# Kernel tuning notes

Measured on AMD Instinct MI355X. Metric: run time of the kernel, lower is better.

Reference implementation:

```python
import jax, jax.numpy as jnp
import numpy as np

B, GRID, D, NF, NC = 4096, 8, 64, 256, 10
N = GRID * GRID          # num_nodes = grid_size**2
LN_EPS = 1e-5            # torch LayerNorm default eps


def _grid_mask():
    m = np.zeros((N, N), np.float32)
    for i in range(N):
        r, c = divmod(i, GRID)
        if r > 0: m[i, i - GRID] = 1
        if r < GRID - 1: m[i, i + GRID] = 1
        if c > 0: m[i, i - 1] = 1
        if c < GRID - 1: m[i, i + 1] = 1
    return jnp.asarray(m)

MASK = _grid_mask()  # static 4-neighbor grid adjacency mask [N,N]


def _ln(x, g, b):
    mu = x.mean(-1, keepdims=True)
    v = ((x - mu) ** 2).mean(-1, keepdims=True)  # biased var, like torch LayerNorm
    return (x - mu) / jnp.sqrt(v + LN_EPS) * g + b


def _regulator(x, h_pre, w_norm, p):
    # HomeostaticRegulator.forward (eval mode: baselines fixed at 0.5 / 1.0)
    var = jnp.var(x, axis=1, ddof=1, keepdims=True)            # torch.var default unbiased=True
    natural_stress = jnp.abs(var - 0.5)
    xs = jnp.sort(x, axis=1)
    smoothness = jnp.abs(xs[:, 1:] - xs[:, :-1]).mean(1, keepdims=True)
    adversarial_stress = jnp.abs(smoothness - 1.0)
    excitation = jnp.abs(h_pre).mean(1, keepdims=True)
    fatigue = jnp.broadcast_to(jnp.reshape(w_norm, (1, 1)), (x.shape[0], 1))
    gradient_proxy = jnp.sqrt((h_pre ** 2).mean(1, keepdims=True))
    s = jnp.concatenate([natural_stress, adversarial_stress, excitation, fatigue, gradient_proxy], axis=1)
    h = jnp.tanh(_ln(s @ p[0].T + p[1], p[2], p[3]))
    h = jnp.tanh(_ln(h @ p[4].T + p[5], p[6], p[7]))
    return jax.nn.sigmoid(h @ p[8].T + p[9])  # [B,3] = metabolism, sensitivity, gate


def _cell(x, W_slow, W_fast, ln_g, ln_b, cp):
    # HomeoContinuumCell.forward, eval mode (no Hebbian buffer update)
    h_raw = jax.lax.stop_gradient(x @ W_slow.T)                 # computed under torch.no_grad
    w_norm = jax.lax.stop_gradient(jnp.sqrt((W_slow ** 2).sum()))
    ctl = _regulator(x, h_raw, w_norm, cp)
    beta = 0.5 + ctl[:, 1:2] * 2.0
    gate = ctl[:, 2:3]
    comb = x @ W_slow.T + (x @ W_fast.T) * gate
    act = comb * jax.nn.sigmoid(beta * comb)
    return _ln(act, ln_g, ln_b)


def _forward(x, W_embed, b_embed, adj_weights, W_slow, W_fast, ln_g, ln_b, W_read, b_read, tp, cp):
    e = x @ W_embed.T + b_embed                                 # [B, N*D]
    e3 = e.reshape(B, N, D)
    # HomeoTopology.get_adjacency with homeostasis (all under no_grad in torch)
    ts = jax.lax.stop_gradient(e.reshape(1, -1))                # flatten whole batch state
    wn = jax.lax.stop_gradient(jnp.sqrt((adj_weights ** 2).sum()))
    ctl = jax.lax.stop_gradient(_regulator(ts, ts, wn, tp))
    ap = ctl[:, 0].mean()                                       # plasticity(=1.0) * mean metabolism
    adj = jax.nn.sigmoid(adj_weights * ap) * MASK
    adj = adj / jnp.clip(adj.sum(1, keepdims=True), 1e-6, None)
    m = jnp.einsum('nm,bmd->bnd', adj, e3)                      # grid message passing
    proc = _cell(m.reshape(B * N, D), W_slow, W_fast, ln_g, ln_b, cp)
    return proc.reshape(B, N * D) @ W_read.T + b_read           # logits [B, NC]


def _reg_params(key, scale=0.2):
    ks = jax.random.split(key, 3)
    return (jax.random.normal(ks[0], (16, 5)) * scale, jnp.zeros(16), jnp.ones(16), jnp.zeros(16),
            jax.random.normal(ks[1], (8, 16)) * scale, jnp.zeros(8), jnp.ones(8), jnp.zeros(8),
            jax.random.normal(ks[2], (3, 8)) * scale, jnp.zeros(3))


def setup_inputs() -> dict:
    key = jax.random.key(0)
    ks = jax.random.split(key, 9)
    inp = {
        'x': jax.random.normal(ks[0], (B, NF)),
        'W_embed': jax.random.normal(ks[1], (N * D, NF)) * (1.0 / np.sqrt(NF)),
        'b_embed': jnp.zeros(N * D),
        'adj_weights': jax.random.normal(ks[2], (N, N)) * 0.1,
        'W_slow': jax.random.normal(ks[3], (D, D)) * (1.4 / np.sqrt(D)),
        'W_fast': jax.random.normal(ks[4], (D, D)) * 0.05,
        'ln_g': jnp.ones(D), 'ln_b': jnp.zeros(D),
        'W_read': jax.random.normal(ks[5], (NC, N * D)) * (1.0 / np.sqrt(N * D)),
        'b_read': jnp.zeros(NC),
    }
    names = ['W1', 'b1', 'g1', 'bb1', 'W2', 'b2', 'g2', 'bb2', 'W3', 'b3']
    for pre, k in (('t', ks[6]), ('c', ks[7])):
        for n, v in zip(names, _reg_params(k)):
            inp[pre + '_' + n] = v
    return inp


def reference(x, W_embed, b_embed, adj_weights, W_slow, W_fast, ln_g, ln_b, W_read, b_read,
              t_W1, t_b1, t_g1, t_bb1, t_W2, t_b2, t_g2, t_bb2, t_W3, t_b3,
              c_W1, c_b1, c_g1, c_bb1, c_W2, c_b2, c_g2, c_bb2, c_W3, c_b3):
    tp = (t_W1, t_b1, t_g1, t_bb1, t_W2, t_b2, t_g2, t_bb2, t_W3, t_b3)
    cp = (c_W1, c_b1, c_g1, c_bb1, c_W2, c_b2, c_g2, c_bb2, c_W3, c_b3)
    return _forward(x, W_embed, b_embed, adj_weights, W_slow, W_fast, ln_g, ln_b, W_read, b_read, tp, cp)
```

## Files before the change

### kernel.cpp

```cpp
#include <hip/hip_runtime.h>

typedef unsigned short u16;
typedef unsigned int   u32;
typedef float f32x4 __attribute__((ext_vector_type(4)));
typedef int   i32x4 __attribute__((ext_vector_type(4)));
typedef int   i32x2 __attribute__((ext_vector_type(2)));
typedef short s8v   __attribute__((ext_vector_type(8)));

__device__ inline u16 f2bf(float f) {
  u32 u = __float_as_uint(f);
  return (u16)((u + 0x7FFFu + ((u >> 16) & 1u)) >> 16);
}
__device__ inline float bf2f(u16 h) { return __uint_as_float(((u32)h) << 16); }

__device__ inline u32 fkey(float f) {
  u32 u = __float_as_uint(f);
  return (u & 0x80000000u) ? ~u : (u | 0x80000000u);
}
__device__ inline float unkey(u32 k) {
  u32 u = (k & 0x80000000u) ? (k & 0x7FFFFFFFu) : ~k;
  return __uint_as_float(u);
}
__device__ inline float fast_tanh(float x) {
  float cx = fminf(fmaxf(x, -15.f), 15.f);
  float e = __expf(2.f * cx);
  return __fdividef(e - 1.f, e + 1.f);
}
__device__ inline float sigm(float x) { return __fdividef(1.f, 1.f + __expf(-x)); }

__device__ inline void gload_lds16(const u16* g, u16* l) {
  __builtin_amdgcn_global_load_lds((const __attribute__((address_space(1))) u32*)g,
                                   (__attribute__((address_space(3))) u32*)l, 16, 0, 0);
}

struct MlpP { const float *W1,*b1,*g1,*bb1,*W2,*b2,*g2,*bb2,*W3,*b3; };

__device__ inline void mlp_eval(const MlpP& p, const float* s, float* ctl) {
  float h1[16];
  float mu = 0.f;
  #pragma unroll
  for (int i = 0; i < 16; ++i) {
    float v = p.b1[i];
    #pragma unroll
    for (int k = 0; k < 5; ++k) v = fmaf(p.W1[i*5+k], s[k], v);
    h1[i] = v; mu += v;
  }
  mu *= (1.0f/16.0f);
  float vv = 0.f;
  #pragma unroll
  for (int i = 0; i < 16; ++i) { float d = h1[i]-mu; vv += d*d; }
  vv *= (1.0f/16.0f);
  float inv = 1.0f/sqrtf(vv + 1e-5f);
  #pragma unroll
  for (int i = 0; i < 16; ++i) h1[i] = fast_tanh((h1[i]-mu)*inv*p.g1[i] + p.bb1[i]);
  float h2[8];
  mu = 0.f;
  #pragma unroll
  for (int o = 0; o < 8; ++o) {
    float v = p.b2[o];
    #pragma unroll
    for (int i = 0; i < 16; ++i) v = fmaf(p.W2[o*16+i], h1[i], v);
    h2[o] = v; mu += v;
  }
  mu *= 0.125f;
  vv = 0.f;
  #pragma unroll
  for (int o = 0; o < 8; ++o) { float d = h2[o]-mu; vv += d*d; }
  vv *= 0.125f;
  inv = 1.0f/sqrtf(vv + 1e-5f);
  #pragma unroll
  for (int o = 0; o < 8; ++o) h2[o] = fast_tanh((h2[o]-mu)*inv*p.g2[o] + p.bb2[o]);
  #pragma unroll
  for (int c = 0; c < 3; ++c) {
    float v = p.b3[c];
    #pragma unroll
    for (int o = 0; o < 8; ++o) v = fmaf(p.W3[c*8+o], h2[o], v);
    ctl[c] = sigm(v);
  }
}

__global__ __launch_bounds__(256) void k_pre(const float* __restrict__ x,
                                             const float* __restrict__ We,
                                             const float* __restrict__ Ws,
                                             const float* __restrict__ Wf,
                                             u16* __restrict__ Xb, u16* __restrict__ Wb,
                                             u16* __restrict__ WsB, u16* __restrict__ WfB,
                                             float* __restrict__ S) {
  const int bi = blockIdx.x, t = threadIdx.x;
  if (bi < 2048) {
    const float* src = (bi < 1024) ? x : We;
    u16* dst = (bi < 1024) ? Xb : Wb;
    int i = ((bi & 1023) * 256 + t) * 4;
    f32x4 v = *(const f32x4*)(src + i);
    u16 o[4] = { f2bf(v[0]), f2bf(v[1]), f2bf(v[2]), f2bf(v[3]) };
    *(u32*)(dst + i)     = ((u32)o[1] << 16) | o[0];
    *(u32*)(dst + i + 2) = ((u32)o[3] << 16) | o[2];
  } else {
    #pragma unroll
    for (int m = 0; m < 2; ++m) {
      const float* src = m ? Wf : Ws;
      u16* dst = m ? WfB : WsB;
      int base = t * 16;
      u16 o[16];
      #pragma unroll
      for (int r = 0; r < 4; ++r) {
        f32x4 v = *(const f32x4*)(src + base + r*4);
        o[r*4+0]=f2bf(v[0]); o[r*4+1]=f2bf(v[1]); o[r*4+2]=f2bf(v[2]); o[r*4+3]=f2bf(v[3]);
      }
      #pragma unroll
      for (int r = 0; r < 8; ++r)
        *(u32*)(dst + base + r*2) = ((u32)o[r*2+1] << 16) | o[r*2];
    }
    if (t < 3) S[t] = 0.f;
    if (t == 3) ((u32*)S)[3] = 0xFFFFFFFFu;
    if (t == 4) ((u32*)S)[4] = 0u;
  }
}

__global__ __launch_bounds__(256) void k_gemm(const u16* __restrict__ Xb,
                                              const u16* __restrict__ Wb,
                                              const float* __restrict__ bias,
                                              u16* __restrict__ E,
                                              float* __restrict__ S) {
  __shared__ __align__(16) u16 As[2][8192];
  __shared__ __align__(16) u16 Bs[2][8192];
  const int t = threadIdx.x;
  const int wv = t >> 6, lane = t & 63;
  const int wr = wv >> 1, wc = wv & 1;
  const int bid = blockIdx.x;
  const int sw = (bid & 7) * 128 + (bid >> 3);
  const int i0 = (sw >> 5) * 128, j0 = (sw & 31) * 128;
  const int rr = lane & 15, q = lane >> 4;
  const int lrow = lane >> 3, lcol = (lane & 7) * 8;

  f32x4 acc[4][4] = {};
  #pragma unroll
  for (int r = 0; r < 4; ++r) {
    const int row = (r*4 + wv)*8 + lrow;
    gload_lds16(Xb + (size_t)(i0 + row)*256 + lcol, &As[0][(r*4 + wv)*512]);
    gload_lds16(Wb + (size_t)(j0 + row)*256 + lcol, &Bs[0][(r*4 + wv)*512]);
  }
  __syncthreads();
  for (int it = 0; it < 4; ++it) {
    const int cur = it & 1;
    if (it < 3) {
      const int k0 = (it + 1) * 64;
      #pragma unroll
      for (int r = 0; r < 4; ++r) {
        const int row = (r*4 + wv)*8 + lrow;
        gload_lds16(Xb + (size_t)(i0 + row)*256 + k0 + lcol, &As[cur^1][(r*4 + wv)*512]);
        gload_lds16(Wb + (size_t)(j0 + row)*256 + k0 + lcol, &Bs[cur^1][(r*4 + wv)*512]);
      }
    }
    #pragma unroll
    for (int ks = 0; ks < 2; ++ks) {
      s8v a[4], b[4];
      #pragma unroll
      for (int m = 0; m < 4; ++m) a[m] = *(const s8v*)&As[cur][(wr*64 + m*16 + rr)*64 + ks*32 + q*8];
      #pragma unroll
      for (int n = 0; n < 4; ++n) b[n] = *(const s8v*)&Bs[cur][(wc*64 + n*16 + rr)*64 + ks*32 + q*8];
      #pragma unroll
      for (int m = 0; m < 4; ++m)
        #pragma unroll
        for (int n = 0; n < 4; ++n)
          acc[m][n] = __builtin_amdgcn_mfma_f32_16x16x32_bf16(a[m], b[n], acc[m][n], 0, 0, 0);
    }
    __syncthreads();
  }
  float s = 0.f, ss = 0.f, sa = 0.f, mnv = 1e30f, mxv = -1e30f;
  #pragma unroll
  for (int n = 0; n < 4; ++n) {
    const int col = j0 + wc*64 + n*16 + rr;
    const float bv = bias[col];
    #pragma unroll
    for (int m = 0; m < 4; ++m) {
      const int rowb = i0 + wr*64 + m*16 + q*4;
      #pragma unroll
      for (int r = 0; r < 4; ++r) {
        float v = acc[m][n][r] + bv;
        E[(size_t)(rowb + r)*4096 + col] = f2bf(v);
        s += v; ss = fmaf(v, v, ss); sa += fabsf(v);
        mnv = fminf(mnv, v); mxv = fmaxf(mxv, v);
      }
    }
  }
  #pragma unroll
  for (int off = 32; off; off >>= 1) {
    s += __shfl_xor(s, off); ss += __shfl_xor(ss, off); sa += __shfl_xor(sa, off);
    mnv = fminf(mnv, __shfl_xor(mnv, off));
    mxv = fmaxf(mxv, __shfl_xor(mxv, off));
  }
  __shared__ float red5[4][5];
  if (lane == 0) { red5[wv][0]=s; red5[wv][1]=ss; red5[wv][2]=sa; red5[wv][3]=mnv; red5[wv][4]=mxv; }
  __syncthreads();
  if (t == 0) {
    float S0 = red5[0][0]+red5[1][0]+red5[2][0]+red5[3][0];
    float S1 = red5[0][1]+red5[1][1]+red5[2][1]+red5[3][1];
    float S2 = red5[0][2]+red5[1][2]+red5[2][2]+red5[3][2];
    float Mn = fminf(fminf(red5[0][3],red5[1][3]), fminf(red5[2][3],red5[3][3]));
    float Mx = fmaxf(fmaxf(red5[0][4],red5[1][4]), fmaxf(red5[2][4],red5[3][4]));
    atomicAdd(&S[0], S0); atomicAdd(&S[1], S1); atomicAdd(&S[2], S2);
    atomicMin((u32*)S + 3, fkey(Mn));
    atomicMax((u32*)S + 4, fkey(Mx));
  }
}

__global__ __launch_bounds__(256) void k_prep(const float* __restrict__ adjw,
    const float* __restrict__ Wslow,
    const float* tW1, const float* tb1, const float* tg1, const float* tbb1,
    const float* tW2, const float* tb2, const float* tg2, const float* tbb2,
    const float* tW3, const float* tb3,
    float* __restrict__ S) {
  __shared__ float red[2][256];
  __shared__ float apL;
  const int t = threadIdx.x;
  float a = 0.f, w = 0.f;
  for (int i = t; i < 4096; i += 256) {
    float v = adjw[i]; a = fmaf(v, v, a);
    float u = Wslow[i]; w = fmaf(u, u, w);
  }
  red[0][t] = a; red[1][t] = w;
  __syncthreads();
  for (int sred = 128; sred > 0; sred >>= 1) {
    if (t < sred) { red[0][t] += red[0][t+sred]; red[1][t] += red[1][t+sred]; }
    __syncthreads();
  }
  if (t == 0) {
    float wn_t = sqrtf(red[0][0]);
    float wn_c = sqrtf(red[1][0]);
    S[7] = wn_c;
    const float n = 16777216.0f, n1 = 16777215.0f;
    float sum = S[0], sumsq = S[1], sumabs = S[2];
    float mean = sum / n;
    float var = (sumsq - sum*mean) / n1;
    float mn = unkey(((u32*)S)[3]);
    float mx = unkey(((u32*)S)[4]);
    float sfv[5];
    sfv[0] = fabsf(var - 0.5f);
    sfv[1] = fabsf((mx - mn)/n1 - 1.0f);
    sfv[2] = sumabs / n;
    sfv[3] = wn_t;
    sfv[4] = sqrtf(sumsq / n);
    MlpP p{tW1,tb1,tg1,tbb1,tW2,tb2,tg2,tbb2,tW3,tb3};
    float ctl[3];
    mlp_eval(p, sfv, ctl);
    apL = ctl[0];
    S[6] = ctl[0];
  }
  __syncthreads();
  if (t < 64) {
    const int rr = t >> 3, cc = t & 7;
    const float ap = apL;
    const int nb[4] = { rr>0 ? t-8 : -1, rr<7 ? t+8 : -1, cc>0 ? t-1 : -1, cc<7 ? t+1 : -1 };
    float w4[4]; float rs = 0.f;
    #pragma unroll
    for (int qq = 0; qq < 4; ++qq) {
      w4[qq] = (nb[qq] >= 0) ? sigm(adjw[t*64 + nb[qq]] * ap) : 0.0f;
      rs += w4[qq];
    }
    rs = fmaxf(rs, 1e-6f);
    #pragma unroll
    for (int qq = 0; qq < 4; ++qq) S[8 + t*4 + qq] = w4[qq] / rs;
  }
}

__global__ __launch_bounds__(256, 4) void k_cell(const u16* __restrict__ E,
    const u16* __restrict__ WsB, const u16* __restrict__ WfB,
    const float* __restrict__ lng, const float* __restrict__ lnb,
    const float* __restrict__ Wread, const float* __restrict__ bread,
    const float* __restrict__ S,
    const float* cW1, const float* cb1, const float* cg1, const float* cbb1,
    const float* cW2, const float* cb2, const float* cg2, const float* cbb2,
    const float* cW3, const float* cb3,
    float* __restrict__ out) {
  __shared__ __align__(16) u16 ebM[64][72];
  __shared__ __align__(16) u16 WsH[64][72];
  __shared__ __align__(16) u16 WfH[64][72];
  __shared__ __align__(16) float adjcL[256];
  __shared__ __align__(16) float prm[308];
  __shared__ __align__(16) float lngL[64], lnbL[64];
  __shared__ float wavp[4][10];
  __shared__ float wncL;

  const int t = threadIdx.x;
  const int wv = t >> 6, lane = t & 63;
  const int b = blockIdx.x;
  const u16* Eb = E + (size_t)b * 4096;

  {
    const int row = t >> 2, c16 = (t & 3) * 16;
    *(i32x4*)&ebM[row][c16]     = *(const i32x4*)(Eb  + row*64 + c16);
    *(i32x4*)&ebM[row][c16 + 8] = *(const i32x4*)(Eb  + row*64 + c16 + 8);
    *(i32x4*)&WsH[row][c16]     = *(const i32x4*)(WsB + row*64 + c16);
    *(i32x4*)&WsH[row][c16 + 8] = *(const i32x4*)(WsB + row*64 + c16 + 8);
    *(i32x4*)&WfH[row][c16]     = *(const i32x4*)(WfB + row*64 + c16);
    *(i32x4*)&WfH[row][c16 + 8] = *(const i32x4*)(WfB + row*64 + c16 + 8);
  }
  adjcL[t] = S[8 + t];
  for (int i = t; i < 80;  i += 256) prm[i] = cW1[i];
  if (t < 16) { prm[80+t]=cb1[t]; prm[96+t]=cg1[t]; prm[112+t]=cbb1[t]; }
  for (int i = t; i < 128; i += 256) prm[128+i] = cW2[i];
  if (t < 8)  { prm[256+t]=cb2[t]; prm[264+t]=cg2[t]; prm[272+t]=cbb2[t]; }
  if (t < 24) prm[280+t] = cW3[t];
  if (t < 3)  prm[304+t] = cb3[t];
  if (t < 64) { lngL[t] = lng[t]; lnbL[t] = lnb[t]; }
  if (t == 0) wncL = S[7];
  __syncthreads();

  float macc[16];
  {
    const int d = lane;
    #pragma unroll
    for (int i = 0; i < 16; ++i) {
      const int n = wv*16 + i;
      const int gr = n >> 3, gc = n & 7;
      const int nb0 = gr > 0 ? n - 8 : 0;
      const int nb1 = gr < 7 ? n + 8 : 0;
      const int nb2 = gc > 0 ? n - 1 : 0;
      const int nb3 = gc < 7 ? n + 1 : 0;
      macc[i] = adjcL[n*4+0]*bf2f(ebM[nb0][d]) + adjcL[n*4+1]*bf2f(ebM[nb1][d])
              + adjcL[n*4+2]*bf2f(ebM[nb2][d]) + adjcL[n*4+3]*bf2f(ebM[nb3][d]);
    }
  }
  __syncthreads();
  #pragma unroll
  for (int i = 0; i < 16; ++i) ebM[wv*16 + i][lane] = f2bf(macc[i]);
  __syncthreads();

  const int rr = lane & 15, q = lane >> 4;
  const int n = wv*16 + rr;
  s8v bm0 = *(const s8v*)&ebM[n][q*8];
  s8v bm1 = *(const s8v*)&ebM[n][32 + q*8];
  f32x4 hs[4], hf[4];
  #pragma unroll
  for (int jt = 0; jt < 4; ++jt) {
    const u16* wsr = &WsH[jt*16 + rr][0];
    const u16* wfr = &WfH[jt*16 + rr][0];
    s8v aw0 = *(const s8v*)(wsr + q*8), aw1 = *(const s8v*)(wsr + 32 + q*8);
    s8v af0 = *(const s8v*)(wfr + q*8), af1 = *(const s8v*)(wfr + 32 + q*8);
    f32x4 z = {0.f, 0.f, 0.f, 0.f};
    hs[jt] = __builtin_amdgcn_mfma_f32_16x16x32_bf16(aw0, bm0, z, 0, 0, 0);
    hs[jt] = __builtin_amdgcn_mfma_f32_16x16x32_bf16(aw1, bm1, hs[jt], 0, 0, 0);
    hf[jt] = __builtin_amdgcn_mfma_f32_16x16x32_bf16(af0, bm0, z, 0, 0, 0);
    hf[jt] = __builtin_amdgcn_mfma_f32_16x16x32_bf16(af1, bm1, hf[jt], 0, 0, 0);
  }

  float s1 = 0.f, s2 = 0.f, mnv = 1e30f, mxv = -1e30f;
  #pragma unroll
  for (int j = 0; j < 8; ++j) {
    float v0 = bf2f((u16)bm0[j]), v1 = bf2f((u16)bm1[j]);
    s1 += v0 + v1;
    s2 = fmaf(v0, v0, s2); s2 = fmaf(v1, v1, s2);
    mnv = fminf(mnv, fminf(v0, v1));
    mxv = fmaxf(mxv, fmaxf(v0, v1));
  }
  float sa = 0.f, sq = 0.f;
  #pragma unroll
  for (int jt = 0; jt < 4; ++jt)
    #pragma unroll
    for (int r = 0; r < 4; ++r) { float v = hs[jt][r]; sa += fabsf(v); sq = fmaf(v, v, sq); }
  #pragma unroll
  for (int off = 16; off <= 32; off <<= 1) {
    s1 += __shfl_xor(s1, off); s2 += __shfl_xor(s2, off);
    sa += __shfl_xor(sa, off); sq += __shfl_xor(sq, off);
    mnv = fminf(mnv, __shfl_xor(mnv, off));
    mxv = fmaxf(mxv, __shfl_xor(mxv, off));
  }
  if (q == 0) {
    float var = (s2 - s1*s1*(1.f/64.f)) * (1.f/63.f);
    f32x4 sv = { fabsf(var - 0.5f),
                 fabsf((mxv - mnv)*(1.f/63.f) - 1.f),
                 sa * (1.f/64.f),
                 sqrtf(sq * (1.f/64.f)) };
    *(f32x4*)&ebM[n][64] = sv;
  }
  __syncthreads();

  if (t < 64) {
    f32x4 sv = *(const f32x4*)&ebM[t][64];
    float sfv[5] = { sv[0], sv[1], sv[2], wncL, sv[3] };
    MlpP p{prm, prm+80, prm+96, prm+112, prm+128, prm+256, prm+264, prm+272, prm+280, prm+304};
    float ctl[3];
    mlp_eval(p, sfv, ctl);
    float* pad = (float*)&ebM[t][64];
    pad[0] = 0.5f + 2.f*ctl[1];
    pad[1] = ctl[2];
  }
  __syncthreads();

  const float beta = ((const float*)&ebM[n][64])[0];
  const float gate = ((const float*)&ebM[n][64])[1];
  float acts[4][4];
  float a1 = 0.f, a2 = 0.f;
  #pragma unroll
  for (int jt = 0; jt < 4; ++jt)
    #pragma unroll
    for (int r = 0; r < 4; ++r) {
      float comb = fmaf(hf[jt][r], gate, hs[jt][r]);
      float sv = comb * sigm(beta * comb);
      acts[jt][r] = sv;
      a1 += sv; a2 = fmaf(sv, sv, a2);
    }
  a1 += __shfl_xor(a1, 16); a2 += __shfl_xor(a2, 16);
  a1 += __shfl_xor(a1, 32); a2 += __shfl_xor(a2, 32);
  float mu = a1 * (1.f/64.f);
  float vvv = a2 * (1.f/64.f) - mu*mu;
  float inv = 1.f / sqrtf(vvv + 1e-5f);
  float racc[10];
  #pragma unroll
  for (int c = 0; c < 10; ++c) racc[c] = 0.f;
  #pragma unroll
  for (int jt = 0; jt < 4; ++jt) {
    f32x4 gv = *(const f32x4*)&lngL[jt*16 + q*4];
    f32x4 bv = *(const f32x4*)&lnbL[jt*16 + q*4];
    float pr[4];
    #pragma unroll
    for (int r = 0; r < 4; ++r) pr[r] = (acts[jt][r] - mu)*inv*gv[r] + bv[r];
    const float* wrb = Wread + n*64 + jt*16 + q*4;
    #pragma unroll
    for (int c = 0; c < 10; ++c) {
      f32x4 w = *(const f32x4*)(wrb + c*4096);
      racc[c] += pr[0]*w[0] + pr[1]*w[1] + pr[2]*w[2] + pr[3]*w[3];
    }
  }
  #pragma unroll
  for (int c = 0; c < 10; ++c) {
    float v = racc[c];
    #pragma unroll
    for (int off = 1; off < 64; off <<= 1) v += __shfl_xor(v, off);
    if (lane == 0) wavp[wv][c] = v;
  }
  __syncthreads();
  if (t < 10) out[(size_t)b*10 + t] = bread[t] + wavp[0][t] + wavp[1][t] + wavp[2][t] + wavp[3][t];
}

extern "C" void kernel_launch(void* const* d_in, const int* in_sizes, int n_in,
                              void* d_out, int out_size, void* d_ws, size_t ws_size,
                              hipStream_t stream) {
  (void)in_sizes; (void)n_in; (void)out_size; (void)ws_size;
  const float* x       = (const float*)d_in[0];
  const float* W_embed = (const float*)d_in[1];
  const float* b_embed = (const float*)d_in[2];
  const float* adjw    = (const float*)d_in[3];
  const float* Wslow   = (const float*)d_in[4];
  const float* Wfast   = (const float*)d_in[5];
  const float* lng     = (const float*)d_in[6];
  const float* lnb     = (const float*)d_in[7];
  const float* Wread   = (const float*)d_in[8];
  const float* bread   = (const float*)d_in[9];
  float* out = (float*)d_out;

  char* ws = (char*)d_ws;
  u16*   Ebf  = (u16*)ws;
  u16*   Xbf  = (u16*)(ws + 33554432);
  u16*   Wbf  = (u16*)(ws + 35651584);
  float* S    = (float*)(ws + 37748736);
  u16*   WsBf = (u16*)(ws + 37752832);
  u16*   WfBf = (u16*)(ws + 37761024);

  hipLaunchKernelGGL(k_pre, dim3(2049), dim3(256), 0, stream,
                     x, W_embed, Wslow, Wfast, Xbf, Wbf, WsBf, WfBf, S);
  hipLaunchKernelGGL(k_gemm, dim3(1024), dim3(256), 0, stream, Xbf, Wbf, b_embed, Ebf, S);
  hipLaunchKernelGGL(k_prep, dim3(1), dim3(256), 0, stream, adjw, Wslow,
                     (const float*)d_in[10], (const float*)d_in[11], (const float*)d_in[12], (const float*)d_in[13],
                     (const float*)d_in[14], (const float*)d_in[15], (const float*)d_in[16], (const float*)d_in[17],
                     (const float*)d_in[18], (const float*)d_in[19], S);
  hipLaunchKernelGGL(k_cell, dim3(4096), dim3(256), 0, stream, Ebf, WsBf, WfBf, lng, lnb,
                     Wread, bread, S,
                     (const float*)d_in[20], (const float*)d_in[21], (const float*)d_in[22], (const float*)d_in[23],
                     (const float*)d_in[24], (const float*)d_in[25], (const float*)d_in[26], (const float*)d_in[27],
                     (const float*)d_in[28], (const float*)d_in[29], out);
}
```

Baseline: 338.8 us.

## Shrink embed GEMM tile to 64x64 with full-K single-stage LDS load

The embedding GEMM moves from 128x128 tiles with a double-buffered K loop fed by global_load_lds to 64x64 tiles. Each block now loads the whole K=256 slab into padded LDS with plain vector loads, then runs all MFMAs after one barrier, and the grid grows from 1024 to 4096 blocks. The aim is more blocks in flight, fewer barriers and fewer LDS bank conflicts thanks to the padding. The cost is twice the global traffic per output element, no overlap between loads and compute, and four times as many partial-statistic reductions into S. The k_cell launch bound also drops its min-blocks hint of 4, which changes register allocation.

Result: slower. 510.7 us (+50.7%).

```diff
diff --git a/kernel.cpp b/kernel.cpp
--- a/kernel.cpp
+++ b/kernel.cpp
@@ -27,11 +27,6 @@
   return __fdividef(e - 1.f, e + 1.f);
 }
 __device__ inline float sigm(float x) { return __fdividef(1.f, 1.f + __expf(-x)); }
-
-__device__ inline void gload_lds16(const u16* g, u16* l) {
-  __builtin_amdgcn_global_load_lds((const __attribute__((address_space(1))) u32*)g,
-                                   (__attribute__((address_space(3))) u32*)l, 16, 0, 0);
-}
 
 struct MlpP { const float *W1,*b1,*g1,*bb1,*W2,*b2,*g2,*bb2,*W3,*b3; };
 
@@ -122,59 +117,50 @@
                                               const float* __restrict__ bias,
                                               u16* __restrict__ E,
                                               float* __restrict__ S) {
-  __shared__ __align__(16) u16 As[2][8192];
-  __shared__ __align__(16) u16 Bs[2][8192];
+  __shared__ __align__(16) u16 As[64*264];
+  __shared__ __align__(16) u16 Bs[64*264];
   const int t = threadIdx.x;
   const int wv = t >> 6, lane = t & 63;
   const int wr = wv >> 1, wc = wv & 1;
   const int bid = blockIdx.x;
-  const int sw = (bid & 7) * 128 + (bid >> 3);
-  const int i0 = (sw >> 5) * 128, j0 = (sw & 31) * 128;
+  const int sw = (bid & 7) * 512 + (bid >> 3);
+  const int i0 = (sw >> 6) * 64, j0 = (sw & 63) * 64;
   const int rr = lane & 15, q = lane >> 4;
-  const int lrow = lane >> 3, lcol = (lane & 7) * 8;
-
-  f32x4 acc[4][4] = {};
-  #pragma unroll
-  for (int r = 0; r < 4; ++r) {
-    const int row = (r*4 + wv)*8 + lrow;
-    gload_lds16(Xb + (size_t)(i0 + row)*256 + lcol, &As[0][(r*4 + wv)*512]);
-    gload_lds16(Wb + (size_t)(j0 + row)*256 + lcol, &Bs[0][(r*4 + wv)*512]);
-  }
-  __syncthreads();
-  for (int it = 0; it < 4; ++it) {
-    const int cur = it & 1;
-    if (it < 3) {
-      const int k0 = (it + 1) * 64;
+
+  #pragma unroll
+  for (int k = 0; k < 8; ++k) {
+    const int e = (k*256 + t) * 8;
+    const int row = e >> 8, col = e & 255;
+    i32x4 va = *(const i32x4*)(Xb + (size_t)(i0 + row)*256 + col);
+    i32x4 vb = *(const i32x4*)(Wb + (size_t)(j0 + row)*256 + col);
+    *(i32x4*)&As[row*264 + col] = va;
+    *(i32x4*)&Bs[row*264 + col] = vb;
+  }
+  __syncthreads();
+
+  f32x4 acc[2][2] = {};
+  #pragma unroll
+  for (int ks = 0; ks < 8; ++ks) {
+    s8v a[2], b[2];
+    a[0] = *(const s8v*)&As[(wr*32 +      rr)*264 + ks*32 + q*8];
+    a[1] = *(const s8v*)&As[(wr*32 + 16 + rr)*264 + ks*32 + q*8];
+    b[0] = *(const s8v*)&Bs[(wc*32 +      rr)*264 + ks*32 + q*8];
+    b[1] = *(const s8v*)&Bs[(wc*32 + 16 + rr)*264 + ks*32 + q*8];
+    #pragma unroll
+    for (int m = 0; m < 2; ++m)
       #pragma unroll
-      for (int r = 0; r < 4; ++r) {
-        const int row = (r*4 + wv)*8 + lrow;
-        gload_lds16(Xb + (size_t)(i0 + row)*256 + k0 + lcol, &As[cur^1][(r*4 + wv)*512]);
-        gload_lds16(Wb + (size_t)(j0 + row)*256 + k0 + lcol, &Bs[cur^1][(r*4 + wv)*512]);
-      }
-    }
-    #pragma unroll
-    for (int ks = 0; ks < 2; ++ks) {
-      s8v a[4], b[4];
-      #pragma unroll
-      for (int m = 0; m < 4; ++m) a[m] = *(const s8v*)&As[cur][(wr*64 + m*16 + rr)*64 + ks*32 + q*8];
-      #pragma unroll
-      for (int n = 0; n < 4; ++n) b[n] = *(const s8v*)&Bs[cur][(wc*64 + n*16 + rr)*64 + ks*32 + q*8];
-      #pragma unroll
-      for (int m = 0; m < 4; ++m)
-        #pragma unroll
-        for (int n = 0; n < 4; ++n)
-          acc[m][n] = __builtin_amdgcn_mfma_f32_16x16x32_bf16(a[m], b[n], acc[m][n], 0, 0, 0);
-    }
-    __syncthreads();
-  }
+      for (int n = 0; n < 2; ++n)
+        acc[m][n] = __builtin_amdgcn_mfma_f32_16x16x32_bf16(a[m], b[n], acc[m][n], 0, 0, 0);
+  }
+
   float s = 0.f, ss = 0.f, sa = 0.f, mnv = 1e30f, mxv = -1e30f;
   #pragma unroll
-  for (int n = 0; n < 4; ++n) {
-    const int col = j0 + wc*64 + n*16 + rr;
+  for (int n = 0; n < 2; ++n) {
+    const int col = j0 + wc*32 + n*16 + rr;
     const float bv = bias[col];
     #pragma unroll
-    for (int m = 0; m < 4; ++m) {
-      const int rowb = i0 + wr*64 + m*16 + q*4;
+    for (int m = 0; m < 2; ++m) {
+      const int rowb = i0 + wr*32 + m*16 + q*4;
       #pragma unroll
       for (int r = 0; r < 4; ++r) {
         float v = acc[m][n][r] + bv;
@@ -264,7 +250,7 @@
   }
 }
 
-__global__ __launch_bounds__(256, 4) void k_cell(const u16* __restrict__ E,
+__global__ __launch_bounds__(256) void k_cell(const u16* __restrict__ E,
     const u16* __restrict__ WsB, const u16* __restrict__ WfB,
     const float* __restrict__ lng, const float* __restrict__ lnb,
     const float* __restrict__ Wread, const float* __restrict__ bread,
@@ -460,7 +446,7 @@
 
   hipLaunchKernelGGL(k_pre, dim3(2049), dim3(256), 0, stream,
                      x, W_embed, Wslow, Wfast, Xbf, Wbf, WsBf, WfBf, S);
-  hipLaunchKernelGGL(k_gemm, dim3(1024), dim3(256), 0, stream, Xbf, Wbf, b_embed, Ebf, S);
+  hipLaunchKernelGGL(k_gemm, dim3(4096), dim3(256), 0, stream, Xbf, Wbf, b_embed, Ebf, S);
   hipLaunchKernelGGL(k_prep, dim3(1), dim3(256), 0, stream, adjw, Wslow,
                      (const float*)d_in[10], (const float*)d_in[11], (const float*)d_in[12], (const float*)d_in[13],
                      (const float*)d_in[14], (const float*)d_in[15], (const float*)d_in[16], (const float*)d_in[17],
```

## Eliminate single-block prep kernel by fusing norms into pre and MLP into cell

Applied to the files above, without the earlier changes.

Removes the one-block k_prep launch. The adjacency and W_slow norm reductions move into the extra block of k_pre, and every k_cell block now recomputes the temporal regulator MLP and the normalized neighbor weights itself. Separately, the GEMM drops its LDS double buffering in favour of a single buffer with a sync after each load, and k_cell loses its occupancy hint of four blocks per CU. This saves a serialized tiny launch but adds redundant per-block work and extra shared memory, and the GEMM loses its load/compute overlap.

After: 349.4 us. 3.1% more time.

```diff
diff --git a/kernel.cpp b/kernel.cpp
--- a/kernel.cpp
+++ b/kernel.cpp
@@ -83,6 +83,7 @@
                                              const float* __restrict__ We,
                                              const float* __restrict__ Ws,
                                              const float* __restrict__ Wf,
+                                             const float* __restrict__ adjw,
                                              u16* __restrict__ Xb, u16* __restrict__ Wb,
                                              u16* __restrict__ WsB, u16* __restrict__ WfB,
                                              float* __restrict__ S) {
@@ -111,6 +112,19 @@
       for (int r = 0; r < 8; ++r)
         *(u32*)(dst + base + r*2) = ((u32)o[r*2+1] << 16) | o[r*2];
     }
+    __shared__ float red2[2][256];
+    float a = 0.f, w = 0.f;
+    for (int i = t; i < 4096; i += 256) {
+      float v = adjw[i]; a = fmaf(v, v, a);
+      float u = Ws[i];   w = fmaf(u, u, w);
+    }
+    red2[0][t] = a; red2[1][t] = w;
+    __syncthreads();
+    for (int sred = 128; sred > 0; sred >>= 1) {
+      if (t < sred) { red2[0][t] += red2[0][t+sred]; red2[1][t] += red2[1][t+sred]; }
+      __syncthreads();
+    }
+    if (t == 0) { S[5] = sqrtf(red2[0][0]); S[7] = sqrtf(red2[1][0]); }
     if (t < 3) S[t] = 0.f;
     if (t == 3) ((u32*)S)[3] = 0xFFFFFFFFu;
     if (t == 4) ((u32*)S)[4] = 0u;
@@ -122,8 +136,8 @@
                                               const float* __restrict__ bias,
                                               u16* __restrict__ E,
                                               float* __restrict__ S) {
-  __shared__ __align__(16) u16 As[2][8192];
-  __shared__ __align__(16) u16 Bs[2][8192];
+  __shared__ __align__(16) u16 As[128*64];
+  __shared__ __align__(16) u16 Bs[128*64];
   const int t = threadIdx.x;
   const int wv = t >> 6, lane = t & 63;
   const int wr = wv >> 1, wc = wv & 1;
@@ -132,33 +146,22 @@
   const int i0 = (sw >> 5) * 128, j0 = (sw & 31) * 128;
   const int rr = lane & 15, q = lane >> 4;
   const int lrow = lane >> 3, lcol = (lane & 7) * 8;
-
   f32x4 acc[4][4] = {};
-  #pragma unroll
-  for (int r = 0; r < 4; ++r) {
-    const int row = (r*4 + wv)*8 + lrow;
-    gload_lds16(Xb + (size_t)(i0 + row)*256 + lcol, &As[0][(r*4 + wv)*512]);
-    gload_lds16(Wb + (size_t)(j0 + row)*256 + lcol, &Bs[0][(r*4 + wv)*512]);
-  }
-  __syncthreads();
-  for (int it = 0; it < 4; ++it) {
-    const int cur = it & 1;
-    if (it < 3) {
-      const int k0 = (it + 1) * 64;
-      #pragma unroll
-      for (int r = 0; r < 4; ++r) {
-        const int row = (r*4 + wv)*8 + lrow;
-        gload_lds16(Xb + (size_t)(i0 + row)*256 + k0 + lcol, &As[cur^1][(r*4 + wv)*512]);
-        gload_lds16(Wb + (size_t)(j0 + row)*256 + k0 + lcol, &Bs[cur^1][(r*4 + wv)*512]);
-      }
-    }
+  for (int k0 = 0; k0 < 256; k0 += 64) {
+    #pragma unroll
+    for (int r = 0; r < 4; ++r) {
+      const int row = (r*4 + wv)*8 + lrow;
+      gload_lds16(Xb + (size_t)(i0 + row)*256 + k0 + lcol, &As[(r*4 + wv)*512]);
+      gload_lds16(Wb + (size_t)(j0 + row)*256 + k0 + lcol, &Bs[(r*4 + wv)*512]);
+    }
+    __syncthreads();
     #pragma unroll
     for (int ks = 0; ks < 2; ++ks) {
       s8v a[4], b[4];
       #pragma unroll
-      for (int m = 0; m < 4; ++m) a[m] = *(const s8v*)&As[cur][(wr*64 + m*16 + rr)*64 + ks*32 + q*8];
-      #pragma unroll
-      for (int n = 0; n < 4; ++n) b[n] = *(const s8v*)&Bs[cur][(wc*64 + n*16 + rr)*64 + ks*32 + q*8];
+      for (int m = 0; m < 4; ++m) a[m] = *(const s8v*)&As[(wr*64 + m*16 + rr)*64 + ks*32 + q*8];
+      #pragma unroll
+      for (int n = 0; n < 4; ++n) b[n] = *(const s8v*)&Bs[(wc*64 + n*16 + rr)*64 + ks*32 + q*8];
       #pragma unroll
       for (int m = 0; m < 4; ++m)
         #pragma unroll
@@ -205,70 +208,15 @@
   }
 }
 
-__global__ __launch_bounds__(256) void k_prep(const float* __restrict__ adjw,
-    const float* __restrict__ Wslow,
+__global__ __launch_bounds__(256) void k_cell(const u16* __restrict__ E,
+    const u16* __restrict__ WsB, const u16* __restrict__ WfB,
+    const float* __restrict__ adjw,
+    const float* __restrict__ lng, const float* __restrict__ lnb,
+    const float* __restrict__ Wread, const float* __restrict__ bread,
+    const float* __restrict__ S,
     const float* tW1, const float* tb1, const float* tg1, const float* tbb1,
     const float* tW2, const float* tb2, const float* tg2, const float* tbb2,
     const float* tW3, const float* tb3,
-    float* __restrict__ S) {
-  __shared__ float red[2][256];
-  __shared__ float apL;
-  const int t = threadIdx.x;
-  float a = 0.f, w = 0.f;
-  for (int i = t; i < 4096; i += 256) {
-    float v = adjw[i]; a = fmaf(v, v, a);
-    float u = Wslow[i]; w = fmaf(u, u, w);
-  }
-  red[0][t] = a; red[1][t] = w;
-  __syncthreads();
-  for (int sred = 128; sred > 0; sred >>= 1) {
-    if (t < sred) { red[0][t] += red[0][t+sred]; red[1][t] += red[1][t+sred]; }
-    __syncthreads();
-  }
-  if (t == 0) {
-    float wn_t = sqrtf(red[0][0]);
-    float wn_c = sqrtf(red[1][0]);
-    S[7] = wn_c;
-    const float n = 16777216.0f, n1 = 16777215.0f;
-    float sum = S[0], sumsq = S[1], sumabs = S[2];
-    float mean = sum / n;
-    float var = (sumsq - sum*mean) / n1;
-    float mn = unkey(((u32*)S)[3]);
-    float mx = unkey(((u32*)S)[4]);
-    float sfv[5];
-    sfv[0] = fabsf(var - 0.5f);
-    sfv[1] = fabsf((mx - mn)/n1 - 1.0f);
-    sfv[2] = sumabs / n;
-    sfv[3] = wn_t;
-    sfv[4] = sqrtf(sumsq / n);
-    MlpP p{tW1,tb1,tg1,tbb1,tW2,tb2,tg2,tbb2,tW3,tb3};
-    float ctl[3];
-    mlp_eval(p, sfv, ctl);
-    apL = ctl[0];
-    S[6] = ctl[0];
-  }
-  __syncthreads();
-  if (t < 64) {
-    const int rr = t >> 3, cc = t & 7;
-    const float ap = apL;
-    const int nb[4] = { rr>0 ? t-8 : -1, rr<7 ? t+8 : -1, cc>0 ? t-1 : -1, cc<7 ? t+1 : -1 };
-    float w4[4]; float rs = 0.f;
-    #pragma unroll
-    for (int qq = 0; qq < 4; ++qq) {
-      w4[qq] = (nb[qq] >= 0) ? sigm(adjw[t*64 + nb[qq]] * ap) : 0.0f;
-      rs += w4[qq];
-    }
-    rs = fmaxf(rs, 1e-6f);
-    #pragma unroll
-    for (int qq = 0; qq < 4; ++qq) S[8 + t*4 + qq] = w4[qq] / rs;
-  }
-}
-
-__global__ __launch_bounds__(256, 4) void k_cell(const u16* __restrict__ E,
-    const u16* __restrict__ WsB, const u16* __restrict__ WfB,
-    const float* __restrict__ lng, const float* __restrict__ lnb,
-    const float* __restrict__ Wread, const float* __restrict__ bread,
-    const float* __restrict__ S,
     const float* cW1, const float* cb1, const float* cg1, const float* cbb1,
     const float* cW2, const float* cb2, const float* cg2, const float* cbb2,
     const float* cW3, const float* cb3,
@@ -278,9 +226,10 @@
   __shared__ __align__(16) u16 WfH[64][72];
   __shared__ __align__(16) float adjcL[256];
   __shared__ __align__(16) float prm[308];
+  __shared__ __align__(16) float tprm[308];
   __shared__ __align__(16) float lngL[64], lnbL[64];
   __shared__ float wavp[4][10];
-  __shared__ float wncL;
+  __shared__ float wncL, apS;
 
   const int t = threadIdx.x;
   const int wv = t >> 6, lane = t & 63;
@@ -296,15 +245,52 @@
     *(i32x4*)&WfH[row][c16]     = *(const i32x4*)(WfB + row*64 + c16);
     *(i32x4*)&WfH[row][c16 + 8] = *(const i32x4*)(WfB + row*64 + c16 + 8);
   }
-  adjcL[t] = S[8 + t];
-  for (int i = t; i < 80;  i += 256) prm[i] = cW1[i];
-  if (t < 16) { prm[80+t]=cb1[t]; prm[96+t]=cg1[t]; prm[112+t]=cbb1[t]; }
-  for (int i = t; i < 128; i += 256) prm[128+i] = cW2[i];
-  if (t < 8)  { prm[256+t]=cb2[t]; prm[264+t]=cg2[t]; prm[272+t]=cbb2[t]; }
-  if (t < 24) prm[280+t] = cW3[t];
-  if (t < 3)  prm[304+t] = cb3[t];
+  for (int i = t; i < 80;  i += 256) { prm[i] = cW1[i]; tprm[i] = tW1[i]; }
+  if (t < 16) { prm[80+t]=cb1[t]; prm[96+t]=cg1[t]; prm[112+t]=cbb1[t];
+                tprm[80+t]=tb1[t]; tprm[96+t]=tg1[t]; tprm[112+t]=tbb1[t]; }
+  for (int i = t; i < 128; i += 256) { prm[128+i] = cW2[i]; tprm[128+i] = tW2[i]; }
+  if (t < 8)  { prm[256+t]=cb2[t]; prm[264+t]=cg2[t]; prm[272+t]=cbb2[t];
+                tprm[256+t]=tb2[t]; tprm[264+t]=tg2[t]; tprm[272+t]=tbb2[t]; }
+  if (t < 24) { prm[280+t] = cW3[t]; tprm[280+t] = tW3[t]; }
+  if (t < 3)  { prm[304+t] = cb3[t]; tprm[304+t] = tb3[t]; }
   if (t < 64) { lngL[t] = lng[t]; lnbL[t] = lnb[t]; }
   if (t == 0) wncL = S[7];
+  __syncthreads();
+
+  if (t == 0) {
+    const float n = 16777216.0f, n1 = 16777215.0f;
+    float sum = S[0], sumsq = S[1], sumabs = S[2];
+    float mean = sum / n;
+    float var = (sumsq - sum*mean) / n1;
+    float mn = unkey(((const u32*)S)[3]);
+    float mx = unkey(((const u32*)S)[4]);
+    float sfv[5];
+    sfv[0] = fabsf(var - 0.5f);
+    sfv[1] = fabsf((mx - mn)/n1 - 1.0f);
+    sfv[2] = sumabs / n;
+    sfv[3] = S[5];
+    sfv[4] = sqrtf(sumsq / n);
+    MlpP p{tprm, tprm+80, tprm+96, tprm+112, tprm+128, tprm+256, tprm+264, tprm+272, tprm+280, tprm+304};
+    float ctl[3];
+    mlp_eval(p, sfv, ctl);
+    apS = ctl[0];
+  }
+  __syncthreads();
+
+  if (t < 64) {
+    const int gr = t >> 3, gc = t & 7;
+    const float ap = apS;
+    const int nb[4] = { gr>0 ? t-8 : -1, gr<7 ? t+8 : -1, gc>0 ? t-1 : -1, gc<7 ? t+1 : -1 };
+    float w4[4]; float rs = 0.f;
+    #pragma unroll
+    for (int qq = 0; qq < 4; ++qq) {
+      w4[qq] = (nb[qq] >= 0) ? sigm(adjw[t*64 + nb[qq]] * ap) : 0.0f;
+      rs += w4[qq];
+    }
+    rs = fmaxf(rs, 1e-6f);
+    #pragma unroll
+    for (int qq = 0; qq < 4; ++qq) adjcL[t*4 + qq] = w4[qq] / rs;
+  }
   __syncthreads();
 
   float macc[16];
@@ -459,14 +445,13 @@
   u16*   WfBf = (u16*)(ws + 37761024);
 
   hipLaunchKernelGGL(k_pre, dim3(2049), dim3(256), 0, stream,
-                     x, W_embed, Wslow, Wfast, Xbf, Wbf, WsBf, WfBf, S);
+                     x, W_embed, Wslow, Wfast, adjw, Xbf, Wbf, WsBf, WfBf, S);
   hipLaunchKernelGGL(k_gemm, dim3(1024), dim3(256), 0, stream, Xbf, Wbf, b_embed, Ebf, S);
-  hipLaunchKernelGGL(k_prep, dim3(1), dim3(256), 0, stream, adjw, Wslow,
+  hipLaunchKernelGGL(k_cell, dim3(4096), dim3(256), 0, stream, Ebf, WsBf, WfBf, adjw,
+                     lng, lnb, Wread, bread, S,
                      (const float*)d_in[10], (const float*)d_in[11], (const float*)d_in[12], (const float*)d_in[13],
                      (const float*)d_in[14], (const float*)d_in[15], (const float*)d_in[16], (const float*)d_in[17],
-                     (const float*)d_in[18], (const float*)d_in[19], S);
-  hipLaunchKernelGGL(k_cell, dim3(4096), dim3(256), 0, stream, Ebf, WsBf, WfBf, lng, lnb,
-                     Wread, bread, S,
+                     (const float*)d_in[18], (const float*)d_in[19],
                      (const float*)d_in[20], (const float*)d_in[21], (const float*)d_in[22], (const float*)d_in[23],
                      (const float*)d_in[24], (const float*)d_in[25], (const float*)d_in[26], (const float*)d_in[27],
                      (const float*)d_in[28], (const float*)d_in[29], out);
```
